# Optimization experiments

Hardware: AMD Instinct MI355X
Metric: run time of the kernel (lower is better)

The kernel has to match this reference:

```python
import jax, jax.numpy as jnp
import numpy as np

B, A, C, M = 16, 76725, 8, 32
EPS = 1e-4


def _iou(b1, b2):
    # b1: [A,4], b2: [M,4]; +1 pixel convention as in the torch source
    lt = jnp.maximum(b1[:, None, :2], b2[None, :, :2])
    rb = jnp.minimum(b1[:, None, 2:], b2[None, :, 2:])
    wh = jnp.clip(rb - lt + 1.0, 0.0)
    inter = wh[..., 0] * wh[..., 1]
    a1 = (b1[:, 2] - b1[:, 0] + 1.0) * (b1[:, 3] - b1[:, 1] + 1.0)
    a2 = (b2[:, 2] - b2[:, 0] + 1.0) * (b2[:, 3] - b2[:, 1] + 1.0)
    return inter / (a1[:, None] + a2[None, :] - inter)


def setup_inputs() -> dict:
    key = jax.random.key(0)
    k1, k2, k3, k4, k5, k6, k7, k8, k9 = jax.random.split(key, 9)
    # anchors: one shared set of boxes, tiled over batch (as RetinaNet does)
    acx = jax.random.uniform(k1, (A,)) * 480.0 + 16.0
    acy = jax.random.uniform(k2, (A,)) * 480.0 + 16.0
    aw = jax.random.uniform(k3, (A,)) * 96.0 + 16.0
    ah = jax.random.uniform(k4, (A,)) * 96.0 + 16.0
    anchor = jnp.stack([acx - 0.5 * aw, acy - 0.5 * ah, acx + 0.5 * aw, acy + 0.5 * ah], -1)
    anchors = jnp.tile(anchor[None], (B, 1, 1))
    # annotations: [B,M,5] = (x1,y1,x2,y2,label); last 8 per image padded with label -1
    x1 = jax.random.uniform(k5, (B, M)) * 380.0
    y1 = jax.random.uniform(k6, (B, M)) * 380.0
    w = jax.random.uniform(k7, (B, M)) * 80.0 + 20.0
    h = jax.random.uniform(k8, (B, M)) * 80.0 + 20.0
    lab = jax.random.randint(k9, (B, M), 0, C).astype(jnp.float32)
    lab = jnp.where(jnp.arange(M)[None, :] < M - 8, lab, -1.0)
    annotations = jnp.stack([x1, y1, x1 + w, y1 + h, lab], -1)
    kc, kr = jax.random.split(jax.random.fold_in(key, 7))
    classifications = jax.random.uniform(kc, (B, A, C), dtype=jnp.float32)
    regressions = jax.random.normal(kr, (B, A, 4), dtype=jnp.float32) * 0.1
    return {
        "classifications": classifications,
        "regressions": regressions,
        "anchors": anchors,
        "annotations": annotations,
    }


def reference(classifications, regressions, anchors, annotations):
    ALPHA, GAMMA = 0.25, 2.0
    dt = classifications.dtype
    nclass = classifications.shape[-1]
    # anchor geometry taken from anchors[0] (as in the torch source)
    anchor0 = anchors[0]
    aw = anchor0[:, 2] - anchor0[:, 0]
    ah = anchor0[:, 3] - anchor0[:, 1]
    acx = anchor0[:, 0] + 0.5 * aw
    acy = anchor0[:, 1] + 0.5 * ah
    norm = jnp.array([0.1, 0.1, 0.2, 0.2], dt)

    def per_image(cls_, reg, anch, ann):
        valid = ann[:, 4] > -0.5  # label != -1
        num_valid = valid.sum()
        iou = _iou(anch, ann[:, :4])  # [A,M]
        iou = jnp.where(valid[None, :], iou, -1.0)  # mask padded annotations
        iou_max = iou.max(axis=1)
        iou_arg = iou.argmax(axis=1)
        p = jnp.clip(cls_, EPS, 1.0 - EPS)  # [A,C]
        assigned = ann[iou_arg]  # [A,5] gather of best annotation per anchor
        pos = iou_max >= 0.4
        npos = pos.sum()
        one_hot = jax.nn.one_hot(assigned[:, 4].astype(jnp.int32), nclass, dtype=dt)
        # targets: -1 ignore, 0 negative (IoU<0.3), one-hot positive (IoU>=0.4)
        targets = jnp.where(pos[:, None], one_hot,
                            jnp.where((iou_max < 0.3)[:, None], 0.0, -1.0))
        is_one = targets == 1.0
        alpha_factor = jnp.where(is_one, ALPHA, 1.0 - ALPHA)
        focal_w = alpha_factor * jnp.where(is_one, 1.0 - p, p) ** GAMMA
        bce = -(targets * jnp.log(p) + (1.0 - targets) * jnp.log1p(-p))
        cls_loss = jnp.where(targets != -1.0, focal_w * bce, 0.0).sum() \
            / jnp.maximum(npos.astype(dt), 1.0)
        w0 = assigned[:, 2] - assigned[:, 0]
        h0 = assigned[:, 3] - assigned[:, 1]
        gcx = assigned[:, 0] + 0.5 * w0
        gcy = assigned[:, 1] + 0.5 * h0
        gw = jnp.clip(w0, 1.0)
        gh = jnp.clip(h0, 1.0)
        t = jnp.stack([(gcx - acx) / aw, (gcy - acy) / ah,
                       jnp.log(gw / aw), jnp.log(gh / ah)], -1) / norm  # [A,4]
        diff = jnp.abs(t - reg)
        sl1 = jnp.where(diff <= 1.0 / 9.0, 0.5 * 9.0 * diff ** 2, diff - 0.5 / 9.0)
        reg_sum = jnp.where(pos[:, None], sl1, 0.0).sum()
        reg_loss = jnp.where(npos > 0,
                             reg_sum / jnp.maximum(npos * 4, 1).astype(dt), 0.0)
        cls_loss = jnp.where(num_valid > 0, cls_loss, 0.0)
        reg_loss = jnp.where(num_valid > 0, reg_loss, 0.0)
        return cls_loss, reg_loss

    cl, rl = jax.vmap(per_image)(classifications, regressions, anchors, annotations)
    return jnp.mean(cl, keepdims=True), jnp.mean(rl, keepdims=True)
```

## Files before the change

kernel.cpp:

```cpp
#include <hip/hip_runtime.h>

#define NB 16
#define NA 76725
#define NC 8
#define NM 32
#define FEPS 1e-4f
#define TPB 256
#define SEQ 4
#define ANCH_PER_BLK (TPB * SEQ)
#define NBLK_X ((NA + ANCH_PER_BLK - 1) / ANCH_PER_BLK)

#define WS_ACC 0
#define WS_NVP (NB * 16)
#define WS_CNT (WS_NVP + 16)
#define WS_REC (WS_CNT + 16)
#define WS_EPI (WS_REC + NB * NM * 8)

__global__ __launch_bounds__(64) void focal_prep(
    const float* __restrict__ ann_, float* __restrict__ ws)
{
    const int b = blockIdx.x;
    const int m = threadIdx.x;
    if (m < 16) ws[WS_ACC + b * 16 + m] = 0.f;
    bool valid = false;
    float x1 = 0.f, y1 = 0.f, x2 = 0.f, y2 = 0.f, lab = -1.f;
    if (m < NM) {
        const float* r = ann_ + ((size_t)b * NM + m) * 5;
        x1 = r[0]; y1 = r[1]; x2 = r[2]; y2 = r[3]; lab = r[4];
        valid = lab > -0.5f;
        float* rec = ws + WS_REC + ((size_t)b * NM + m) * 8;
        rec[0] = 3e18f; rec[1] = 3e18f; rec[2] = -3e18f; rec[3] = -3e18f;
        rec[4] = 1.0f;  rec[5] = -1.f;  rec[6] = 0.f;    rec[7] = 0.f;
        reinterpret_cast<float4*>(ws + WS_EPI)[b * NM + m] = make_float4(0.f, 0.f, 0.f, 0.f);
    }
    const unsigned long long mask = __ballot(valid);
    const int cnt = __popcll(mask);
    __syncthreads();
    if (valid) {
        const int idx = __popcll(mask & ((1ull << m) - 1ull));
        float* rec = ws + WS_REC + ((size_t)b * NM + idx) * 8;
        rec[0] = x1; rec[1] = y1; rec[2] = x2 + 1.f; rec[3] = y2 + 1.f;
        rec[4] = (x2 - x1 + 1.f) * (y2 - y1 + 1.f);
        rec[5] = lab;
        const float w0 = x2 - x1, h0 = y2 - y1;
        reinterpret_cast<float4*>(ws + WS_EPI)[b * NM + idx] =
            make_float4(x1 + 0.5f * w0, y1 + 0.5f * h0,
                        __logf(fmaxf(w0, 1.f)), __logf(fmaxf(h0, 1.f)));
    }
    if (m == 0) {
        ws[WS_CNT + b] = (float)cnt;
        ws[WS_NVP + b] = (float)((cnt + 7) & ~7);
    }
}

__global__ __launch_bounds__(TPB, 4) void focal_main(
    const float* __restrict__ cls_,
    const float* __restrict__ reg_,
    const float* __restrict__ anch_,
    const float* __restrict__ tab,
    float* __restrict__ acc)
{
    const int b   = blockIdx.y;
    const int tid = threadIdx.x;

    const float4* __restrict__ anch4 = reinterpret_cast<const float4*>(anch_);
    const float4* __restrict__ reg4  = reinterpret_cast<const float4*>(reg_);
    const float4* __restrict__ cls4  = reinterpret_cast<const float4*>(cls_);

    const int ab = blockIdx.x * ANCH_PER_BLK + tid;
    bool mk0, mk1, mk2, mk3;
    auto addr = [&](int s, bool& msk) -> size_t {
        const int a = ab + s * TPB;
        msk = (a < NA);
        return (size_t)b * NA + (msk ? a : (NA - 1));
    };

    const size_t b0 = addr(0, mk0);
    float4 anA = anch4[b0], rgA = reg4[b0], cv0A = cls4[b0 * 2], cv1A = cls4[b0 * 2 + 1];

    __shared__ float  s_x1[NM], s_y1[NM], s_x21[NM], s_y21[NM], s_a2[NM], s_lab[NM];
    __shared__ float4 s_epi[NM];
    if (tid < NM) {
        const float4 r0 = reinterpret_cast<const float4*>(tab + WS_REC)[(b * NM + tid) * 2];
        const float4 r1 = reinterpret_cast<const float4*>(tab + WS_REC)[(b * NM + tid) * 2 + 1];
        s_x1[tid] = r0.x; s_y1[tid] = r0.y; s_x21[tid] = r0.z; s_y21[tid] = r0.w;
        s_a2[tid] = r1.x; s_lab[tid] = r1.y;
        s_epi[tid] = reinterpret_cast<const float4*>(tab + WS_EPI)[b * NM + tid];
    }
    int nvp = (int)tab[WS_NVP + b];
    nvp = __builtin_amdgcn_readfirstlane(nvp);
    __syncthreads();

    float cls_c = 0.f, reg_c = 0.f;
    unsigned pos_c = 0;

    auto compute = [&](const float4& an, const float4& rg,
                       const float4& cv0, const float4& cv1, bool msk) {
        const float ax = an.x, ay = an.y;
        const float az1 = an.z + 1.f, aw1 = an.w + 1.f;
        const float area1 = (an.z - ax + 1.f) * (an.w - ay + 1.f);

        float ib = 0.f, ub = 1.f;
        int arg = 0;
        #pragma unroll 4
        for (int m = 0; m < nvp; ++m) {
            const float x1 = s_x1[m], y1 = s_y1[m];
            const float x21 = s_x21[m], y21 = s_y21[m];
            const float a2 = s_a2[m];
            const float w = fminf(az1, x21) - fmaxf(ax, x1);
            const float h = fminf(aw1, y21) - fmaxf(ay, y1);
            const float inter = fmaxf(w, 0.f) * fmaxf(h, 0.f);
            const float u = area1 + a2 - inter;
            const bool better = inter * ub > ib * u;
            ib  = better ? inter : ib;
            ub  = better ? u : ub;
            arg = better ? m : arg;
        }
        const bool pos = ib >= 0.4f * ub;
        const bool neg = ib <  0.3f * ub;
        const bool act = (pos || neg) && msk;

        {
            const float pv[8] = {cv0.x, cv0.y, cv0.z, cv0.w, cv1.x, cv1.y, cv1.z, cv1.w};
            float pcl[8];
            float bsum = 0.f;
            #pragma unroll
            for (int c = 0; c < NC; ++c) {
                const float p = fminf(fmaxf(pv[c], FEPS), 1.f - FEPS);
                pcl[c] = p;
                bsum += 0.75f * p * p * (-__logf(1.f - p));
            }
            float contrib = bsum;
            if (pos) {
                const int labi = (int)s_lab[arg];
                const float t0 = (labi & 1) ? pcl[1] : pcl[0];
                const float t1 = (labi & 1) ? pcl[3] : pcl[2];
                const float t2 = (labi & 1) ? pcl[5] : pcl[4];
                const float t3 = (labi & 1) ? pcl[7] : pcl[6];
                const float u0 = (labi & 2) ? t1 : t0;
                const float u1 = (labi & 2) ? t3 : t2;
                const float pt = (labi & 4) ? u1 : u0;
                const float om = 1.f - pt;
                contrib += 0.25f * om * om * (-__logf(pt))
                         - 0.75f * pt * pt * (-__logf(om));
            }
            cls_c += act ? contrib : 0.f;
        }
        if (pos && msk) {
            pos_c += 1;
            const float4 ep = s_epi[arg];
            const float awd = az1 - 1.f - ax;
            const float ahd = aw1 - 1.f - ay;
            const float acx = ax + 0.5f * awd;
            const float acy = ay + 0.5f * ahd;
            const float t0 = __fdividef(ep.x - acx, awd) * 10.f;
            const float t1 = __fdividef(ep.y - acy, ahd) * 10.f;
            const float t2 = (ep.z - __logf(awd)) * 5.f;
            const float t3 = (ep.w - __logf(ahd)) * 5.f;
            const float d0 = fabsf(t0 - rg.x);
            const float d1 = fabsf(t1 - rg.y);
            const float d2 = fabsf(t2 - rg.z);
            const float d3 = fabsf(t3 - rg.w);
            auto sl1 = [](float d) {
                return d <= (1.f / 9.f) ? 4.5f * d * d : d - (0.5f / 9.f);
            };
            reg_c += sl1(d0) + sl1(d1) + sl1(d2) + sl1(d3);
        }
    };

    const size_t b1 = addr(1, mk1);
    float4 anB = anch4[b1], rgB = reg4[b1], cv0B = cls4[b1 * 2], cv1B = cls4[b1 * 2 + 1];
    __builtin_amdgcn_sched_barrier(0);
    compute(anA, rgA, cv0A, cv1A, mk0);

    const size_t b2 = addr(2, mk2);
    anA = anch4[b2]; rgA = reg4[b2]; cv0A = cls4[b2 * 2]; cv1A = cls4[b2 * 2 + 1];
    __builtin_amdgcn_sched_barrier(0);
    compute(anB, rgB, cv0B, cv1B, mk1);

    const size_t b3 = addr(3, mk3);
    anB = anch4[b3]; rgB = reg4[b3]; cv0B = cls4[b3 * 2]; cv1B = cls4[b3 * 2 + 1];
    __builtin_amdgcn_sched_barrier(0);
    compute(anA, rgA, cv0A, cv1A, mk2);

    compute(anB, rgB, cv0B, cv1B, mk3);

    #pragma unroll
    for (int off = 32; off > 0; off >>= 1) {
        cls_c += __shfl_down(cls_c, off);
        reg_c += __shfl_down(reg_c, off);
        pos_c += __shfl_down(pos_c, off);
    }
    __shared__ float    sc[4], sr[4];
    __shared__ unsigned sp[4];
    const int wave = tid >> 6, lane = tid & 63;
    if (lane == 0) { sc[wave] = cls_c; sr[wave] = reg_c; sp[wave] = pos_c; }
    __syncthreads();
    if (tid == 0) {
        const float    c = sc[0] + sc[1] + sc[2] + sc[3];
        const float    r = sr[0] + sr[1] + sr[2] + sr[3];
        const unsigned p = sp[0] + sp[1] + sp[2] + sp[3];
        atomicAdd(&acc[WS_ACC + b * 16 + 0], c);
        atomicAdd(&acc[WS_ACC + b * 16 + 1], r);
        atomicAdd(reinterpret_cast<unsigned*>(acc) + WS_ACC + b * 16 + 2, p);
    }
}

__global__ __launch_bounds__(64) void focal_finalize(
    const float* __restrict__ ws, float* __restrict__ out)
{
    __shared__ float s_cls[NB], s_reg[NB];
    const int b = threadIdx.x;
    if (b < NB) {
        const float    nv      = ws[WS_CNT + b];
        const float    cls_sum = ws[WS_ACC + b * 16 + 0];
        const float    reg_sum = ws[WS_ACC + b * 16 + 1];
        const unsigned npos    = reinterpret_cast<const unsigned*>(ws)[WS_ACC + b * 16 + 2];
        float cl = cls_sum / fmaxf((float)npos, 1.f);
        float rl = (npos > 0u) ? reg_sum / (float)(npos * 4u) : 0.f;
        if (nv < 0.5f) { cl = 0.f; rl = 0.f; }
        s_cls[b] = cl;
        s_reg[b] = rl;
    }
    __syncthreads();
    if (threadIdx.x == 0) {
        float c = 0.f, r = 0.f;
        for (int i = 0; i < NB; ++i) { c += s_cls[i]; r += s_reg[i]; }
        out[0] = c * (1.f / NB);
        out[1] = r * (1.f / NB);
    }
}

extern "C" void kernel_launch(void* const* d_in, const int* in_sizes, int n_in,
                              void* d_out, int out_size, void* d_ws, size_t ws_size,
                              hipStream_t stream)
{
    const float* cls_  = (const float*)d_in[0];
    const float* reg_  = (const float*)d_in[1];
    const float* anch_ = (const float*)d_in[2];
    const float* ann_  = (const float*)d_in[3];
    float* ws  = (float*)d_ws;
    float* out = (float*)d_out;

    focal_prep<<<NB, 64, 0, stream>>>(ann_, ws);
    dim3 grid(NBLK_X, NB);
    focal_main<<<grid, dim3(TPB), 0, stream>>>(cls_, reg_, anch_, ws, ws);
    focal_finalize<<<1, 64, 0, stream>>>(ws, out);
}
```

Before: 41.10 us.

## Fuse annotation prep into main kernel and replace atomics with per-block partials

Removes the separate prep kernel: each main block now compacts the valid annotations for its image straight into shared memory. The global atomics are replaced by per-block float4 partial results that the finalize kernel reduces, which also drops the need to zero the workspace. The anchor split changes to 96 blocks of 800 anchors per image, with the fourth step handled only by the first 32 threads. This saves one kernel launch and the atomic contention, at the cost of each block redoing the small annotation compaction and leaving most lanes idle in the last step.

New measurement: 40.60 us. About the same (-1.2%).

```diff
diff --git a/kernel.cpp b/kernel.cpp
--- a/kernel.cpp
+++ b/kernel.cpp
@@ -6,90 +6,63 @@
 #define NM 32
 #define FEPS 1e-4f
 #define TPB 256
-#define SEQ 4
-#define ANCH_PER_BLK (TPB * SEQ)
-#define NBLK_X ((NA + ANCH_PER_BLK - 1) / ANCH_PER_BLK)
-
-#define WS_ACC 0
-#define WS_NVP (NB * 16)
-#define WS_CNT (WS_NVP + 16)
-#define WS_REC (WS_CNT + 16)
-#define WS_EPI (WS_REC + NB * NM * 8)
-
-__global__ __launch_bounds__(64) void focal_prep(
-    const float* __restrict__ ann_, float* __restrict__ ws)
-{
-    const int b = blockIdx.x;
-    const int m = threadIdx.x;
-    if (m < 16) ws[WS_ACC + b * 16 + m] = 0.f;
-    bool valid = false;
-    float x1 = 0.f, y1 = 0.f, x2 = 0.f, y2 = 0.f, lab = -1.f;
-    if (m < NM) {
-        const float* r = ann_ + ((size_t)b * NM + m) * 5;
-        x1 = r[0]; y1 = r[1]; x2 = r[2]; y2 = r[3]; lab = r[4];
-        valid = lab > -0.5f;
-        float* rec = ws + WS_REC + ((size_t)b * NM + m) * 8;
-        rec[0] = 3e18f; rec[1] = 3e18f; rec[2] = -3e18f; rec[3] = -3e18f;
-        rec[4] = 1.0f;  rec[5] = -1.f;  rec[6] = 0.f;    rec[7] = 0.f;
-        reinterpret_cast<float4*>(ws + WS_EPI)[b * NM + m] = make_float4(0.f, 0.f, 0.f, 0.f);
-    }
-    const unsigned long long mask = __ballot(valid);
-    const int cnt = __popcll(mask);
-    __syncthreads();
-    if (valid) {
-        const int idx = __popcll(mask & ((1ull << m) - 1ull));
-        float* rec = ws + WS_REC + ((size_t)b * NM + idx) * 8;
-        rec[0] = x1; rec[1] = y1; rec[2] = x2 + 1.f; rec[3] = y2 + 1.f;
-        rec[4] = (x2 - x1 + 1.f) * (y2 - y1 + 1.f);
-        rec[5] = lab;
-        const float w0 = x2 - x1, h0 = y2 - y1;
-        reinterpret_cast<float4*>(ws + WS_EPI)[b * NM + idx] =
-            make_float4(x1 + 0.5f * w0, y1 + 0.5f * h0,
-                        __logf(fmaxf(w0, 1.f)), __logf(fmaxf(h0, 1.f)));
-    }
-    if (m == 0) {
-        ws[WS_CNT + b] = (float)cnt;
-        ws[WS_NVP + b] = (float)((cnt + 7) & ~7);
-    }
-}
+#define NBX 96
+#define APB 800
+
 
 __global__ __launch_bounds__(TPB, 4) void focal_main(
     const float* __restrict__ cls_,
     const float* __restrict__ reg_,
     const float* __restrict__ anch_,
-    const float* __restrict__ tab,
-    float* __restrict__ acc)
+    const float* __restrict__ ann_,
+    float4* __restrict__ partial)
 {
     const int b   = blockIdx.y;
+    const int xb  = blockIdx.x;
     const int tid = threadIdx.x;
 
     const float4* __restrict__ anch4 = reinterpret_cast<const float4*>(anch_);
     const float4* __restrict__ reg4  = reinterpret_cast<const float4*>(reg_);
     const float4* __restrict__ cls4  = reinterpret_cast<const float4*>(cls_);
 
-    const int ab = blockIdx.x * ANCH_PER_BLK + tid;
-    bool mk0, mk1, mk2, mk3;
-    auto addr = [&](int s, bool& msk) -> size_t {
-        const int a = ab + s * TPB;
-        msk = (a < NA);
-        return (size_t)b * NA + (msk ? a : (NA - 1));
-    };
-
-    const size_t b0 = addr(0, mk0);
-    float4 anA = anch4[b0], rgA = reg4[b0], cv0A = cls4[b0 * 2], cv1A = cls4[b0 * 2 + 1];
+    const int ab = xb * APB;
+
+    const int a0 = ab + tid;
+    const bool mk0 = (a0 < NA);
+    const size_t b0 = (size_t)b * NA + (mk0 ? a0 : (NA - 1));
+    float4 anA = anch4[b0], rgA = reg4[b0], c0A = cls4[b0 * 2], c1A = cls4[b0 * 2 + 1];
 
     __shared__ float  s_x1[NM], s_y1[NM], s_x21[NM], s_y21[NM], s_a2[NM], s_lab[NM];
     __shared__ float4 s_epi[NM];
-    if (tid < NM) {
-        const float4 r0 = reinterpret_cast<const float4*>(tab + WS_REC)[(b * NM + tid) * 2];
-        const float4 r1 = reinterpret_cast<const float4*>(tab + WS_REC)[(b * NM + tid) * 2 + 1];
-        s_x1[tid] = r0.x; s_y1[tid] = r0.y; s_x21[tid] = r0.z; s_y21[tid] = r0.w;
-        s_a2[tid] = r1.x; s_lab[tid] = r1.y;
-        s_epi[tid] = reinterpret_cast<const float4*>(tab + WS_EPI)[b * NM + tid];
-    }
-    int nvp = (int)tab[WS_NVP + b];
-    nvp = __builtin_amdgcn_readfirstlane(nvp);
+    __shared__ int    s_nvp, s_cnt;
+    if (tid < 64) {
+        bool valid = false;
+        float x1 = 0.f, y1 = 0.f, x2 = 0.f, y2 = 0.f, lab = -1.f;
+        if (tid < NM) {
+            const float* r = ann_ + ((size_t)b * NM + tid) * 5;
+            x1 = r[0]; y1 = r[1]; x2 = r[2]; y2 = r[3]; lab = r[4];
+            valid = lab > -0.5f;
+        }
+        const unsigned long long mask = __ballot(valid);
+        const int cnt = __popcll(mask);
+        if (tid < NM) {
+            s_x1[tid] = 3e18f; s_y1[tid] = 3e18f; s_x21[tid] = -3e18f; s_y21[tid] = -3e18f;
+            s_a2[tid] = 1.f;   s_lab[tid] = -1.f;
+            s_epi[tid] = make_float4(0.f, 0.f, 0.f, 0.f);
+        }
+        if (valid) {
+            const int idx = __popcll(mask & ((1ull << tid) - 1ull));
+            s_x1[idx] = x1; s_y1[idx] = y1; s_x21[idx] = x2 + 1.f; s_y21[idx] = y2 + 1.f;
+            s_a2[idx] = (x2 - x1 + 1.f) * (y2 - y1 + 1.f);
+            s_lab[idx] = lab;
+            const float w0 = x2 - x1, h0 = y2 - y1;
+            s_epi[idx] = make_float4(x1 + 0.5f * w0, y1 + 0.5f * h0,
+                                     __logf(fmaxf(w0, 1.f)), __logf(fmaxf(h0, 1.f)));
+        }
+        if (tid == 0) { s_nvp = (cnt + 7) & ~7; s_cnt = cnt; }
+    }
     __syncthreads();
+    int nvp = __builtin_amdgcn_readfirstlane(s_nvp);
 
     float cls_c = 0.f, reg_c = 0.f;
     unsigned pos_c = 0;
@@ -168,22 +141,30 @@
         }
     };
 
-    const size_t b1 = addr(1, mk1);
-    float4 anB = anch4[b1], rgB = reg4[b1], cv0B = cls4[b1 * 2], cv1B = cls4[b1 * 2 + 1];
+    const int a1 = ab + TPB + tid;
+    const bool mk1 = (a1 < NA);
+    const size_t b1 = (size_t)b * NA + (mk1 ? a1 : (NA - 1));
+    float4 anB = anch4[b1], rgB = reg4[b1], c0B = cls4[b1 * 2], c1B = cls4[b1 * 2 + 1];
     __builtin_amdgcn_sched_barrier(0);
-    compute(anA, rgA, cv0A, cv1A, mk0);
-
-    const size_t b2 = addr(2, mk2);
-    anA = anch4[b2]; rgA = reg4[b2]; cv0A = cls4[b2 * 2]; cv1A = cls4[b2 * 2 + 1];
+    compute(anA, rgA, c0A, c1A, mk0);
+
+    const int a2i = ab + 2 * TPB + tid;
+    const bool mk2 = (a2i < NA);
+    const size_t b2 = (size_t)b * NA + (mk2 ? a2i : (NA - 1));
+    anA = anch4[b2]; rgA = reg4[b2]; c0A = cls4[b2 * 2]; c1A = cls4[b2 * 2 + 1];
     __builtin_amdgcn_sched_barrier(0);
-    compute(anB, rgB, cv0B, cv1B, mk1);
-
-    const size_t b3 = addr(3, mk3);
-    anB = anch4[b3]; rgB = reg4[b3]; cv0B = cls4[b3 * 2]; cv1B = cls4[b3 * 2 + 1];
+    compute(anB, rgB, c0B, c1B, mk1);
+
+    bool mk3 = false;
+    if (tid < 32) {
+        const int a3 = ab + 3 * TPB + tid;
+        mk3 = (a3 < NA);
+        const size_t b3 = (size_t)b * NA + (mk3 ? a3 : (NA - 1));
+        anB = anch4[b3]; rgB = reg4[b3]; c0B = cls4[b3 * 2]; c1B = cls4[b3 * 2 + 1];
+    }
     __builtin_amdgcn_sched_barrier(0);
-    compute(anA, rgA, cv0A, cv1A, mk2);
-
-    compute(anB, rgB, cv0B, cv1B, mk3);
+    compute(anA, rgA, c0A, c1A, mk2);
+    if (tid < 32) compute(anB, rgB, c0B, c1B, mk3);
 
     #pragma unroll
     for (int off = 32; off > 0; off >>= 1) {
@@ -200,34 +181,37 @@
         const float    c = sc[0] + sc[1] + sc[2] + sc[3];
         const float    r = sr[0] + sr[1] + sr[2] + sr[3];
         const unsigned p = sp[0] + sp[1] + sp[2] + sp[3];
-        atomicAdd(&acc[WS_ACC + b * 16 + 0], c);
-        atomicAdd(&acc[WS_ACC + b * 16 + 1], r);
-        atomicAdd(reinterpret_cast<unsigned*>(acc) + WS_ACC + b * 16 + 2, p);
+        partial[b * NBX + xb] = make_float4(c, r, (float)p, (float)s_cnt);
     }
 }
 
 __global__ __launch_bounds__(64) void focal_finalize(
-    const float* __restrict__ ws, float* __restrict__ out)
+    const float4* __restrict__ partial, float* __restrict__ out)
 {
-    __shared__ float s_cls[NB], s_reg[NB];
-    const int b = threadIdx.x;
-    if (b < NB) {
-        const float    nv      = ws[WS_CNT + b];
-        const float    cls_sum = ws[WS_ACC + b * 16 + 0];
-        const float    reg_sum = ws[WS_ACC + b * 16 + 1];
-        const unsigned npos    = reinterpret_cast<const unsigned*>(ws)[WS_ACC + b * 16 + 2];
-        float cl = cls_sum / fmaxf((float)npos, 1.f);
-        float rl = (npos > 0u) ? reg_sum / (float)(npos * 4u) : 0.f;
-        if (nv < 0.5f) { cl = 0.f; rl = 0.f; }
-        s_cls[b] = cl;
-        s_reg[b] = rl;
-    }
-    __syncthreads();
-    if (threadIdx.x == 0) {
-        float c = 0.f, r = 0.f;
-        for (int i = 0; i < NB; ++i) { c += s_cls[i]; r += s_reg[i]; }
-        out[0] = c * (1.f / NB);
-        out[1] = r * (1.f / NB);
+    const int t = threadIdx.x;
+    const int b = t & 15, q = t >> 4;
+    float cs = 0.f, rs = 0.f, np = 0.f;
+    for (int x = q; x < NBX; x += 4) {
+        const float4 v = partial[b * NBX + x];
+        cs += v.x; rs += v.y; np += v.z;
+    }
+    cs += __shfl_down(cs, 32); rs += __shfl_down(rs, 32); np += __shfl_down(np, 32);
+    cs += __shfl_down(cs, 16); rs += __shfl_down(rs, 16); np += __shfl_down(np, 16);
+    float cl = 0.f, rl = 0.f;
+    if (t < 16) {
+        const float cnt = partial[b * NBX].w;
+        cl = cs / fmaxf(np, 1.f);
+        rl = (np > 0.5f) ? rs / (np * 4.f) : 0.f;
+        if (cnt < 0.5f) { cl = 0.f; rl = 0.f; }
+    }
+    #pragma unroll
+    for (int off = 8; off > 0; off >>= 1) {
+        cl += __shfl_down(cl, off);
+        rl += __shfl_down(rl, off);
+    }
+    if (t == 0) {
+        out[0] = cl * (1.f / NB);
+        out[1] = rl * (1.f / NB);
     }
 }
 
@@ -239,11 +223,10 @@
     const float* reg_  = (const float*)d_in[1];
     const float* anch_ = (const float*)d_in[2];
     const float* ann_  = (const float*)d_in[3];
-    float* ws  = (float*)d_ws;
-    float* out = (float*)d_out;
-
-    focal_prep<<<NB, 64, 0, stream>>>(ann_, ws);
-    dim3 grid(NBLK_X, NB);
-    focal_main<<<grid, dim3(TPB), 0, stream>>>(cls_, reg_, anch_, ws, ws);
-    focal_finalize<<<1, 64, 0, stream>>>(ws, out);
+    float4* partial = (float4*)d_ws;
+    float*  out     = (float*)d_out;
+
+    dim3 grid(NBX, NB);
+    focal_main<<<grid, dim3(TPB), 0, stream>>>(cls_, reg_, anch_, ann_, partial);
+    focal_finalize<<<1, 64, 0, stream>>>(partial, out);
 }
```
